# Kernel tuning notes

Measured on AMD Instinct MI355X. Metric: run time of the kernel, lower is better.

Reference implementation:

```python
import jax, jax.numpy as jnp
import numpy as np

N_NODES = 100000
N_EDGES = 1600000
D_IN = 128
D_HID = 128


def setup_inputs() -> dict:
    key = jax.random.key(0)
    ks = jax.random.split(key, 9)
    x = jax.random.normal(ks[0], (N_NODES, D_IN), dtype=jnp.float32)
    edge_index = jax.random.randint(ks[1], (2, N_EDGES), 0, N_NODES, dtype=jnp.int64)
    s = 1.0 / np.sqrt(D_IN)
    W0 = jax.random.uniform(ks[2], (D_IN, D_HID), jnp.float32, -s, s)
    W1 = jax.random.uniform(ks[3], (D_HID, D_HID), jnp.float32, -s, s)
    W2 = jax.random.uniform(ks[4], (D_HID, D_HID), jnp.float32, -s, s)
    b0 = jax.random.uniform(ks[5], (D_HID,), jnp.float32, -s, s)
    b1 = jax.random.uniform(ks[6], (D_HID,), jnp.float32, -s, s)
    b2 = jax.random.uniform(ks[7], (D_HID,), jnp.float32, -s, s)
    return {"x": x, "edge_index": edge_index,
            "W0": W0, "W1": W1, "W2": W2, "b0": b0, "b1": b1, "b2": b2}


def _gcn_norm(edge_index, num_nodes):
    # add self loops, compute symmetric normalization D^-1/2 (A+I) D^-1/2
    loop = jnp.arange(num_nodes, dtype=edge_index.dtype)
    src = jnp.concatenate([edge_index[0], loop])
    dst = jnp.concatenate([edge_index[1], loop])
    deg = jax.ops.segment_sum(jnp.ones_like(dst, dtype=jnp.float32), dst,
                              num_segments=num_nodes)
    dis = jnp.where(deg > 0, jax.lax.rsqrt(deg), 0.0)
    norm = dis[src] * dis[dst]  # [E+N]
    return src, dst, norm


def _gcn_conv(x, src, dst, norm, W, b, num_nodes):
    h = x @ W                           # [N, D]
    msg = h[src] * norm[:, None]        # [E+N, D]
    out = jax.ops.segment_sum(msg, dst, num_segments=num_nodes)
    return out + b


def reference(x, edge_index, W0, W1, W2, b0, b1, b2):
    n = x.shape[0]
    src, dst, norm = _gcn_norm(edge_index, n)
    h = jax.nn.relu(_gcn_conv(x, src, dst, norm, W0, b0, n))
    h = jax.nn.relu(_gcn_conv(h, src, dst, norm, W1, b1, n))
    h = jax.nn.relu(_gcn_conv(h, src, dst, norm, W2, b2, n))
    return jax.nn.log_softmax(h, axis=1)
```

## Files before the change

### kernel.cpp

```cpp
#include <hip/hip_runtime.h>
#include <cstdint>


#define D 128
#define NBMAX 800
#define ACHUNK 8192

typedef __attribute__((ext_vector_type(8))) short bf16x8;
typedef __attribute__((ext_vector_type(4))) float f32x4;

__device__ inline ushort f_to_bf(float f) {
    uint x = __float_as_uint(f);
    return (ushort)((x + 0x7fffu + ((x >> 16) & 1u)) >> 16);
}
__device__ inline uint pack_bf2(float a, float b) {
    return (uint)f_to_bf(a) | ((uint)f_to_bf(b) << 16);
}
__device__ inline float bf_lo(uint u) { return __uint_as_float(u << 16); }
__device__ inline float bf_hi(uint u) { return __uint_as_float(u & 0xffff0000u); }


__global__ void hist_pass(const int* __restrict__ ei, int* __restrict__ hist,
                          int E, int NB) {
    __shared__ int lh[NBMAX];
    for (int i = threadIdx.x; i < NB; i += 256) lh[i] = 0;
    __syncthreads();
    int e0 = blockIdx.x * ACHUNK;
    int e1 = min(e0 + ACHUNK, E);
    for (int e = e0 + threadIdx.x; e < e1; e += 256)
        atomicAdd(&lh[ei[(size_t)E + e] >> 7], 1);
    __syncthreads();
    int* hrow = hist + (size_t)blockIdx.x * NB;
    for (int i = threadIdx.x; i < NB; i += 256) hrow[i] = lh[i];
}

__global__ void col_scan(int* __restrict__ hist, int* __restrict__ btotal,
                         int B, int NB) {
    __shared__ int s[256];
    int g = blockIdx.x;
    int t = threadIdx.x;
    int v = (t < B) ? hist[(size_t)t * NB + g] : 0;
    s[t] = v;
    __syncthreads();
    for (int off = 1; off < 256; off <<= 1) {
        int u = (t >= off) ? s[t - off] : 0;
        __syncthreads();
        s[t] += u;
        __syncthreads();
    }
    if (t < B) hist[(size_t)t * NB + g] = s[t] - v;
    if (t == 255) btotal[g] = s[255];
}

__global__ void base_scan(const int* __restrict__ btotal, int* __restrict__ bbase,
                          int NB, int E) {
    __shared__ int s[1024];
    int t = threadIdx.x;
    int v = (t < NB) ? btotal[t] : 0;
    s[t] = v;
    __syncthreads();
    for (int off = 1; off < 1024; off <<= 1) {
        int u = (t >= off) ? s[t - off] : 0;
        __syncthreads();
        s[t] += u;
        __syncthreads();
    }
    if (t < NB) bbase[t] = s[t] - v;
    if (t == 0) bbase[NB] = E;
}

__global__ void scatter_pass(const int* __restrict__ ei, const int* __restrict__ hist,
                             const int* __restrict__ bbase, uint2* __restrict__ queue,
                             int E, int NB) {
    __shared__ int loff[NBMAX];
    const int* hrow = hist + (size_t)blockIdx.x * NB;
    for (int i = threadIdx.x; i < NB; i += 256) loff[i] = bbase[i] + hrow[i];
    __syncthreads();
    int e0 = blockIdx.x * ACHUNK;
    int e1 = min(e0 + ACHUNK, E);
    for (int e = e0 + threadIdx.x; e < e1; e += 256) {
        int d = ei[(size_t)E + e];
        int s = ei[e];
        int slot = atomicAdd(&loff[d >> 7], 1);
        queue[slot] = make_uint2((uint)d, (uint)s);
    }
}

__global__ void finalize_pass(const uint2* __restrict__ queue, const int* __restrict__ bbase,
                              int* __restrict__ rowptr, float* __restrict__ dis,
                              int* __restrict__ col, int N, int NB) {
    __shared__ int cnt[128], pre[128], run[128];
    int g = blockIdx.x;
    int t = threadIdx.x;
    int base = bbase[g], next = bbase[g + 1];
    if (t < 128) { cnt[t] = 0; run[t] = 0; }
    __syncthreads();
    for (int i = base + t; i < next; i += 256)
        atomicAdd(&cnt[queue[i].x & 127], 1);
    __syncthreads();
    if (t < 128) pre[t] = cnt[t];
    __syncthreads();
    for (int off = 1; off < 128; off <<= 1) {
        int u = (t < 128 && t >= off) ? pre[t - off] : 0;
        __syncthreads();
        if (t < 128) pre[t] += u;
        __syncthreads();
    }
    if (t < 128) {
        int node = (g << 7) + t;
        if (node < N) {
            rowptr[node] = base + pre[t] - cnt[t];
            dis[node] = rsqrtf((float)(cnt[t] + 1));
        }
    }
    if (g == NB - 1 && t == 0) rowptr[N] = next;
    __syncthreads();
    for (int i = base + t; i < next; i += 256) {
        uint2 e = queue[i];
        int idx = (int)(e.x & 127);
        int r = atomicAdd(&run[idx], 1);
        col[base + pre[idx] - cnt[idx] + r] = (int)e.y;
    }
}

__global__ void convert_w3(const float* __restrict__ W0, const float* __restrict__ W1,
                           const float* __restrict__ W2, ushort* __restrict__ Wt0,
                           ushort* __restrict__ Wt1, ushort* __restrict__ Wt2) {
    int which = blockIdx.x >> 6;
    int i = (blockIdx.x & 63) * 256 + threadIdx.x;
    const float* W = which == 0 ? W0 : (which == 1 ? W1 : W2);
    ushort* Wt = which == 0 ? Wt0 : (which == 1 ? Wt1 : Wt2);
    int k = i >> 7, nn = i & 127;
    Wt[nn * D + k] = f_to_bf(W[i]);
}

template <int F32IN>
__global__ __launch_bounds__(256)
void gemm_mfma(const void* __restrict__ Xv, const ushort* __restrict__ Wt,
               const float* __restrict__ dis, ushort* __restrict__ G, int n) {
    __shared__ ushort Bs[32 * 64 * 8];
    int tid = threadIdx.x;
    int wave = tid >> 6, lane = tid & 63;
    int lr = lane & 15, quad = lane >> 4;
    int rowbase = blockIdx.x * 128 + wave * 32;

    for (int s = tid; s < 2048; s += 256) {
        int g = s >> 6, l = s & 63;
        int kk = g >> 3, nt = g & 7;
        int srow = nt * 16 + (l & 15);
        int scol = kk * 32 + (l >> 4) * 8;
        ((uint4*)Bs)[s] = *(const uint4*)(Wt + srow * D + scol);
    }
    __syncthreads();

    int ar0 = min(rowbase + lr, n - 1);
    int ar1 = min(rowbase + 16 + lr, n - 1);

    f32x4 acc[2][8];
#pragma unroll
    for (int rt = 0; rt < 2; rt++)
#pragma unroll
        for (int nt = 0; nt < 8; nt++) acc[rt][nt] = (f32x4){0.f, 0.f, 0.f, 0.f};

#pragma unroll
    for (int kk = 0; kk < 4; kk++) {
        bf16x8 a0, a1;
        if (F32IN) {
            const float* X = (const float*)Xv;
            const float* p0 = X + (size_t)ar0 * D + kk * 32 + quad * 8;
            const float* p1 = X + (size_t)ar1 * D + kk * 32 + quad * 8;
            float4 u0 = ((const float4*)p0)[0], v0 = ((const float4*)p0)[1];
            float4 u1 = ((const float4*)p1)[0], v1 = ((const float4*)p1)[1];
            a0 = (bf16x8){(short)f_to_bf(u0.x), (short)f_to_bf(u0.y), (short)f_to_bf(u0.z), (short)f_to_bf(u0.w),
                          (short)f_to_bf(v0.x), (short)f_to_bf(v0.y), (short)f_to_bf(v0.z), (short)f_to_bf(v0.w)};
            a1 = (bf16x8){(short)f_to_bf(u1.x), (short)f_to_bf(u1.y), (short)f_to_bf(u1.z), (short)f_to_bf(u1.w),
                          (short)f_to_bf(v1.x), (short)f_to_bf(v1.y), (short)f_to_bf(v1.z), (short)f_to_bf(v1.w)};
        } else {
            const ushort* X = (const ushort*)Xv;
            a0 = ((const bf16x8*)(X + (size_t)ar0 * D))[kk * 4 + quad];
            a1 = ((const bf16x8*)(X + (size_t)ar1 * D))[kk * 4 + quad];
        }
#pragma unroll
        for (int nt = 0; nt < 8; nt++) {
            bf16x8 b = ((const bf16x8*)Bs)[(kk * 8 + nt) * 64 + lane];
            acc[0][nt] = __builtin_amdgcn_mfma_f32_16x16x32_bf16(a0, b, acc[0][nt], 0, 0, 0);
            acc[1][nt] = __builtin_amdgcn_mfma_f32_16x16x32_bf16(a1, b, acc[1][nt], 0, 0, 0);
        }
    }

#pragma unroll
    for (int rt = 0; rt < 2; rt++) {
#pragma unroll
        for (int r = 0; r < 4; r++) {
            int row = rowbase + rt * 16 + quad * 4 + r;
            if (row < n) {
                float dsc = dis[row];
#pragma unroll
                for (int nt = 0; nt < 8; nt++)
                    G[(size_t)row * D + nt * 16 + lr] = f_to_bf(dsc * acc[rt][nt][r]);
            }
        }
    }
}

template <int MODE>
__global__ __launch_bounds__(256)
void aggregate(const ushort* __restrict__ Gv, const float* __restrict__ dis,
               const int* __restrict__ rowptr, const int* __restrict__ col,
               const float* __restrict__ bias, void* __restrict__ outv, int n) {
    int node = blockIdx.x * 16 + (threadIdx.x >> 4);
    if (node >= n) return;
    int lane = threadIdx.x & 15;
    const uint4* base = (const uint4*)Gv;

    uint4 u = base[(size_t)node * 16 + lane];
    float a0 = bf_lo(u.x), a1 = bf_hi(u.x), a2 = bf_lo(u.y), a3 = bf_hi(u.y);
    float a4 = bf_lo(u.z), a5 = bf_hi(u.z), a6 = bf_lo(u.w), a7 = bf_hi(u.w);

    int beg = rowptr[node], end = rowptr[node + 1];
    int j = beg;
    for (; j + 8 <= end; j += 8) {
        uint4 v0 = base[(size_t)col[j + 0] * 16 + lane];
        uint4 v1 = base[(size_t)col[j + 1] * 16 + lane];
        uint4 v2 = base[(size_t)col[j + 2] * 16 + lane];
        uint4 v3 = base[(size_t)col[j + 3] * 16 + lane];
        uint4 v4 = base[(size_t)col[j + 4] * 16 + lane];
        uint4 v5 = base[(size_t)col[j + 5] * 16 + lane];
        uint4 v6 = base[(size_t)col[j + 6] * 16 + lane];
        uint4 v7 = base[(size_t)col[j + 7] * 16 + lane];
        a0 += bf_lo(v0.x) + bf_lo(v1.x) + bf_lo(v2.x) + bf_lo(v3.x)
            + bf_lo(v4.x) + bf_lo(v5.x) + bf_lo(v6.x) + bf_lo(v7.x);
        a1 += bf_hi(v0.x) + bf_hi(v1.x) + bf_hi(v2.x) + bf_hi(v3.x)
            + bf_hi(v4.x) + bf_hi(v5.x) + bf_hi(v6.x) + bf_hi(v7.x);
        a2 += bf_lo(v0.y) + bf_lo(v1.y) + bf_lo(v2.y) + bf_lo(v3.y)
            + bf_lo(v4.y) + bf_lo(v5.y) + bf_lo(v6.y) + bf_lo(v7.y);
        a3 += bf_hi(v0.y) + bf_hi(v1.y) + bf_hi(v2.y) + bf_hi(v3.y)
            + bf_hi(v4.y) + bf_hi(v5.y) + bf_hi(v6.y) + bf_hi(v7.y);
        a4 += bf_lo(v0.z) + bf_lo(v1.z) + bf_lo(v2.z) + bf_lo(v3.z)
            + bf_lo(v4.z) + bf_lo(v5.z) + bf_lo(v6.z) + bf_lo(v7.z);
        a5 += bf_hi(v0.z) + bf_hi(v1.z) + bf_hi(v2.z) + bf_hi(v3.z)
            + bf_hi(v4.z) + bf_hi(v5.z) + bf_hi(v6.z) + bf_hi(v7.z);
        a6 += bf_lo(v0.w) + bf_lo(v1.w) + bf_lo(v2.w) + bf_lo(v3.w)
            + bf_lo(v4.w) + bf_lo(v5.w) + bf_lo(v6.w) + bf_lo(v7.w);
        a7 += bf_hi(v0.w) + bf_hi(v1.w) + bf_hi(v2.w) + bf_hi(v3.w)
            + bf_hi(v4.w) + bf_hi(v5.w) + bf_hi(v6.w) + bf_hi(v7.w);
    }
    for (; j < end; j++) {
        uint4 v = base[(size_t)col[j] * 16 + lane];
        a0 += bf_lo(v.x); a1 += bf_hi(v.x); a2 += bf_lo(v.y); a3 += bf_hi(v.y);
        a4 += bf_lo(v.z); a5 += bf_hi(v.z); a6 += bf_lo(v.w); a7 += bf_hi(v.w);
    }

    float di = dis[node];
    float4 bA = ((const float4*)bias)[lane * 2];
    float4 bB = ((const float4*)bias)[lane * 2 + 1];
    a0 = fmaxf(di * a0 + bA.x, 0.f); a1 = fmaxf(di * a1 + bA.y, 0.f);
    a2 = fmaxf(di * a2 + bA.z, 0.f); a3 = fmaxf(di * a3 + bA.w, 0.f);
    a4 = fmaxf(di * a4 + bB.x, 0.f); a5 = fmaxf(di * a5 + bB.y, 0.f);
    a6 = fmaxf(di * a6 + bB.z, 0.f); a7 = fmaxf(di * a7 + bB.w, 0.f);

    if (MODE == 1) {
        float m = fmaxf(fmaxf(fmaxf(a0, a1), fmaxf(a2, a3)),
                        fmaxf(fmaxf(a4, a5), fmaxf(a6, a7)));
        for (int off = 8; off > 0; off >>= 1) m = fmaxf(m, __shfl_xor(m, off, 16));
        float e = __expf(a0 - m) + __expf(a1 - m) + __expf(a2 - m) + __expf(a3 - m)
                + __expf(a4 - m) + __expf(a5 - m) + __expf(a6 - m) + __expf(a7 - m);
        for (int off = 8; off > 0; off >>= 1) e += __shfl_xor(e, off, 16);
        float ls = m + __logf(e);
        ((float4*)outv)[(size_t)node * 32 + lane * 2]     = make_float4(a0 - ls, a1 - ls, a2 - ls, a3 - ls);
        ((float4*)outv)[(size_t)node * 32 + lane * 2 + 1] = make_float4(a4 - ls, a5 - ls, a6 - ls, a7 - ls);
    } else {
        ((uint4*)outv)[(size_t)node * 16 + lane] =
            make_uint4(pack_bf2(a0, a1), pack_bf2(a2, a3), pack_bf2(a4, a5), pack_bf2(a6, a7));
    }
}


static inline size_t align256(size_t x) { return (x + 255) & ~(size_t)255; }

extern "C" void kernel_launch(void* const* d_in, const int* in_sizes, int n_in,
                              void* d_out, int out_size, void* d_ws, size_t ws_size,
                              hipStream_t stream) {
    const float* x  = (const float*)d_in[0];
    const int*   ei = (const int*)d_in[1];
    const float* W0 = (const float*)d_in[2];
    const float* W1 = (const float*)d_in[3];
    const float* W2 = (const float*)d_in[4];
    const float* b0 = (const float*)d_in[5];
    const float* b1 = (const float*)d_in[6];
    const float* b2 = (const float*)d_in[7];
    float* out      = (float*)d_out;

    const int N = in_sizes[0] / D;
    const int E = in_sizes[1] / 2;

    const int NB = (N + 127) >> 7;
    const int B  = (E + ACHUNK - 1) / ACHUNK;

    char* ws = (char*)d_ws;
    size_t off = 0;
    float*  dis      = (float*)(ws + off);  off = align256(off + (size_t)N * 4);
    int*    rowptr   = (int*)(ws + off);    off = align256(off + ((size_t)N + 1) * 4);
    int*    hist     = (int*)(ws + off);    off = align256(off + (size_t)B * NB * 4);
    int*    btotal   = (int*)(ws + off);    off = align256(off + ((size_t)NB + 1) * 4);
    int*    bbase    = (int*)(ws + off);    off = align256(off + ((size_t)NB + 1) * 4);
    ushort* Wt0      = (ushort*)(ws + off); off = align256(off + (size_t)D * D * 2);
    ushort* Wt1      = (ushort*)(ws + off); off = align256(off + (size_t)D * D * 2);
    ushort* Wt2      = (ushort*)(ws + off); off = align256(off + (size_t)D * D * 2);
    int*    col      = (int*)(ws + off);    off = align256(off + (size_t)E * 4);
    ushort* xb       = (ushort*)(ws + off); off = align256(off + (size_t)N * D * 2);
    ushort* gA       = (ushort*)(ws + off); off = align256(off + (size_t)N * D * 2);
    ushort* hb       = (ushort*)d_out;
    uint2*  queue    = (uint2*)gA;
    (void)ws_size;

    hist_pass<<<B, 256, 0, stream>>>(ei, hist, E, NB);
    col_scan<<<NB, 256, 0, stream>>>(hist, btotal, B, NB);
    base_scan<<<1, 1024, 0, stream>>>(btotal, bbase, NB, E);
    scatter_pass<<<B, 256, 0, stream>>>(ei, hist, bbase, queue, E, NB);
    finalize_pass<<<NB, 256, 0, stream>>>(queue, bbase, rowptr, dis, col, N, NB);

    convert_w3<<<192, 256, 0, stream>>>(W0, W1, W2, Wt0, Wt1, Wt2);

    const int gemmBlocks = (N + 127) / 128;
    const int aggBlocks  = (N + 15) / 16;

    gemm_mfma<1><<<gemmBlocks, 256, 0, stream>>>(x, Wt0, dis, gA, N);
    aggregate<0><<<aggBlocks, 256, 0, stream>>>(gA, dis, rowptr, col, b0, hb, N);
    gemm_mfma<0><<<gemmBlocks, 256, 0, stream>>>(hb, Wt1, dis, gA, N);
    aggregate<0><<<aggBlocks, 256, 0, stream>>>(gA, dis, rowptr, col, b1, xb, N);
    gemm_mfma<0><<<gemmBlocks, 256, 0, stream>>>(xb, Wt2, dis, gA, N);
    aggregate<1><<<aggBlocks, 256, 0, stream>>>(gA, dis, rowptr, col, b2, out, N);
}
```

Measured before the change: 414.2 us.

## Build CSR with global atomic degree count and unordered per-node scatter

Replaces the five-kernel bucketed counting sort (histogram, column scan, base scan, bucket scatter, finalize) with three kernels: a global atomic degree count, a block-level scan that claims row ranges by atomic on a global counter, and a direct atomic scatter into col. Row ranges are stored as (begin, degree) pairs, so rows need not be contiguous in node order, and zeroing of the counters is folded into the weight-conversion kernel. This removes launches and the intermediate queue pass. In exchange it adds contention from global atomics, nondeterministic neighbor order within rows, and possibly poorer locality of col reads in aggregation.

```diff
diff --git a/kernel.cpp b/kernel.cpp
--- a/kernel.cpp
+++ b/kernel.cpp
@@ -3,8 +3,6 @@
 
 
 #define D 128
-#define NBMAX 800
-#define ACHUNK 8192
 
 typedef __attribute__((ext_vector_type(8))) short bf16x8;
 typedef __attribute__((ext_vector_type(4))) float f32x4;
@@ -20,27 +18,20 @@
 __device__ inline float bf_hi(uint u) { return __uint_as_float(u & 0xffff0000u); }
 
 
-__global__ void hist_pass(const int* __restrict__ ei, int* __restrict__ hist,
-                          int E, int NB) {
-    __shared__ int lh[NBMAX];
-    for (int i = threadIdx.x; i < NB; i += 256) lh[i] = 0;
-    __syncthreads();
-    int e0 = blockIdx.x * ACHUNK;
-    int e1 = min(e0 + ACHUNK, E);
-    for (int e = e0 + threadIdx.x; e < e1; e += 256)
-        atomicAdd(&lh[ei[(size_t)E + e] >> 7], 1);
-    __syncthreads();
-    int* hrow = hist + (size_t)blockIdx.x * NB;
-    for (int i = threadIdx.x; i < NB; i += 256) hrow[i] = lh[i];
-}
-
-__global__ void col_scan(int* __restrict__ hist, int* __restrict__ btotal,
-                         int B, int NB) {
+__global__ void deg_count(const int* __restrict__ ei, int* __restrict__ cnt, int E) {
+    int stride = gridDim.x * blockDim.x;
+    for (int e = blockIdx.x * blockDim.x + threadIdx.x; e < E; e += stride)
+        atomicAdd(&cnt[ei[(size_t)E + e]], 1);
+}
+
+__global__ void assign_base(int* __restrict__ cnt, int2* __restrict__ bd,
+                            float* __restrict__ dis, int N) {
     __shared__ int s[256];
-    int g = blockIdx.x;
+    __shared__ int base;
     int t = threadIdx.x;
-    int v = (t < B) ? hist[(size_t)t * NB + g] : 0;
-    s[t] = v;
+    int i = blockIdx.x * 256 + t;
+    int d = (i < N) ? cnt[i] : 0;
+    s[t] = d;
     __syncthreads();
     for (int off = 1; off < 256; off <<= 1) {
         int u = (t >= off) ? s[t - off] : 0;
@@ -48,84 +39,33 @@
         s[t] += u;
         __syncthreads();
     }
-    if (t < B) hist[(size_t)t * NB + g] = s[t] - v;
-    if (t == 255) btotal[g] = s[255];
-}
-
-__global__ void base_scan(const int* __restrict__ btotal, int* __restrict__ bbase,
-                          int NB, int E) {
-    __shared__ int s[1024];
-    int t = threadIdx.x;
-    int v = (t < NB) ? btotal[t] : 0;
-    s[t] = v;
+    if (t == 255) base = atomicAdd(&cnt[N], s[255]);
     __syncthreads();
-    for (int off = 1; off < 1024; off <<= 1) {
-        int u = (t >= off) ? s[t - off] : 0;
-        __syncthreads();
-        s[t] += u;
-        __syncthreads();
-    }
-    if (t < NB) bbase[t] = s[t] - v;
-    if (t == 0) bbase[NB] = E;
-}
-
-__global__ void scatter_pass(const int* __restrict__ ei, const int* __restrict__ hist,
-                             const int* __restrict__ bbase, uint2* __restrict__ queue,
-                             int E, int NB) {
-    __shared__ int loff[NBMAX];
-    const int* hrow = hist + (size_t)blockIdx.x * NB;
-    for (int i = threadIdx.x; i < NB; i += 256) loff[i] = bbase[i] + hrow[i];
-    __syncthreads();
-    int e0 = blockIdx.x * ACHUNK;
-    int e1 = min(e0 + ACHUNK, E);
-    for (int e = e0 + threadIdx.x; e < e1; e += 256) {
+    if (i < N) {
+        int beg = base + s[t] - d;
+        bd[i] = make_int2(beg, d);
+        cnt[i] = beg;
+        dis[i] = rsqrtf((float)(d + 1));
+    }
+}
+
+__global__ void scatter_csr(const int* __restrict__ ei, int* __restrict__ cur,
+                            int* __restrict__ col, int E) {
+    int stride = gridDim.x * blockDim.x;
+    for (int e = blockIdx.x * blockDim.x + threadIdx.x; e < E; e += stride) {
         int d = ei[(size_t)E + e];
         int s = ei[e];
-        int slot = atomicAdd(&loff[d >> 7], 1);
-        queue[slot] = make_uint2((uint)d, (uint)s);
-    }
-}
-
-__global__ void finalize_pass(const uint2* __restrict__ queue, const int* __restrict__ bbase,
-                              int* __restrict__ rowptr, float* __restrict__ dis,
-                              int* __restrict__ col, int N, int NB) {
-    __shared__ int cnt[128], pre[128], run[128];
-    int g = blockIdx.x;
-    int t = threadIdx.x;
-    int base = bbase[g], next = bbase[g + 1];
-    if (t < 128) { cnt[t] = 0; run[t] = 0; }
-    __syncthreads();
-    for (int i = base + t; i < next; i += 256)
-        atomicAdd(&cnt[queue[i].x & 127], 1);
-    __syncthreads();
-    if (t < 128) pre[t] = cnt[t];
-    __syncthreads();
-    for (int off = 1; off < 128; off <<= 1) {
-        int u = (t < 128 && t >= off) ? pre[t - off] : 0;
-        __syncthreads();
-        if (t < 128) pre[t] += u;
-        __syncthreads();
-    }
-    if (t < 128) {
-        int node = (g << 7) + t;
-        if (node < N) {
-            rowptr[node] = base + pre[t] - cnt[t];
-            dis[node] = rsqrtf((float)(cnt[t] + 1));
-        }
-    }
-    if (g == NB - 1 && t == 0) rowptr[N] = next;
-    __syncthreads();
-    for (int i = base + t; i < next; i += 256) {
-        uint2 e = queue[i];
-        int idx = (int)(e.x & 127);
-        int r = atomicAdd(&run[idx], 1);
-        col[base + pre[idx] - cnt[idx] + r] = (int)e.y;
+        int slot = atomicAdd(&cur[d], 1);
+        col[slot] = s;
     }
 }
 
 __global__ void convert_w3(const float* __restrict__ W0, const float* __restrict__ W1,
                            const float* __restrict__ W2, ushort* __restrict__ Wt0,
-                           ushort* __restrict__ Wt1, ushort* __restrict__ Wt2) {
+                           ushort* __restrict__ Wt1, ushort* __restrict__ Wt2,
+                           int* __restrict__ cnt, int N) {
+    int gid = blockIdx.x * 256 + threadIdx.x;
+    for (int z = gid; z <= N; z += 192 * 256) cnt[z] = 0;
     int which = blockIdx.x >> 6;
     int i = (blockIdx.x & 63) * 256 + threadIdx.x;
     const float* W = which == 0 ? W0 : (which == 1 ? W1 : W2);
@@ -206,7 +146,7 @@
 template <int MODE>
 __global__ __launch_bounds__(256)
 void aggregate(const ushort* __restrict__ Gv, const float* __restrict__ dis,
-               const int* __restrict__ rowptr, const int* __restrict__ col,
+               const int2* __restrict__ bd, const int* __restrict__ col,
                const float* __restrict__ bias, void* __restrict__ outv, int n) {
     int node = blockIdx.x * 16 + (threadIdx.x >> 4);
     if (node >= n) return;
@@ -217,7 +157,8 @@
     float a0 = bf_lo(u.x), a1 = bf_hi(u.x), a2 = bf_lo(u.y), a3 = bf_hi(u.y);
     float a4 = bf_lo(u.z), a5 = bf_hi(u.z), a6 = bf_lo(u.w), a7 = bf_hi(u.w);
 
-    int beg = rowptr[node], end = rowptr[node + 1];
+    int2 be = bd[node];
+    int beg = be.x, end = be.x + be.y;
     int j = beg;
     for (; j + 8 <= end; j += 8) {
         uint4 v0 = base[(size_t)col[j + 0] * 16 + lane];
@@ -294,16 +235,11 @@
     const int N = in_sizes[0] / D;
     const int E = in_sizes[1] / 2;
 
-    const int NB = (N + 127) >> 7;
-    const int B  = (E + ACHUNK - 1) / ACHUNK;
-
     char* ws = (char*)d_ws;
     size_t off = 0;
     float*  dis      = (float*)(ws + off);  off = align256(off + (size_t)N * 4);
-    int*    rowptr   = (int*)(ws + off);    off = align256(off + ((size_t)N + 1) * 4);
-    int*    hist     = (int*)(ws + off);    off = align256(off + (size_t)B * NB * 4);
-    int*    btotal   = (int*)(ws + off);    off = align256(off + ((size_t)NB + 1) * 4);
-    int*    bbase    = (int*)(ws + off);    off = align256(off + ((size_t)NB + 1) * 4);
+    int*    cnt      = (int*)(ws + off);    off = align256(off + ((size_t)N + 1) * 4);
+    int2*   bd       = (int2*)(ws + off);   off = align256(off + (size_t)N * 8);
     ushort* Wt0      = (ushort*)(ws + off); off = align256(off + (size_t)D * D * 2);
     ushort* Wt1      = (ushort*)(ws + off); off = align256(off + (size_t)D * D * 2);
     ushort* Wt2      = (ushort*)(ws + off); off = align256(off + (size_t)D * D * 2);
@@ -311,24 +247,21 @@
     ushort* xb       = (ushort*)(ws + off); off = align256(off + (size_t)N * D * 2);
     ushort* gA       = (ushort*)(ws + off); off = align256(off + (size_t)N * D * 2);
     ushort* hb       = (ushort*)d_out;
-    uint2*  queue    = (uint2*)gA;
     (void)ws_size;
 
-    hist_pass<<<B, 256, 0, stream>>>(ei, hist, E, NB);
-    col_scan<<<NB, 256, 0, stream>>>(hist, btotal, B, NB);
-    base_scan<<<1, 1024, 0, stream>>>(btotal, bbase, NB, E);
-    scatter_pass<<<B, 256, 0, stream>>>(ei, hist, bbase, queue, E, NB);
-    finalize_pass<<<NB, 256, 0, stream>>>(queue, bbase, rowptr, dis, col, N, NB);
-
-    convert_w3<<<192, 256, 0, stream>>>(W0, W1, W2, Wt0, Wt1, Wt2);
+    convert_w3<<<192, 256, 0, stream>>>(W0, W1, W2, Wt0, Wt1, Wt2, cnt, N);
+
+    deg_count<<<1024, 256, 0, stream>>>(ei, cnt, E);
+    assign_base<<<(N + 255) / 256, 256, 0, stream>>>(cnt, bd, dis, N);
+    scatter_csr<<<2048, 256, 0, stream>>>(ei, cnt, col, E);
 
     const int gemmBlocks = (N + 127) / 128;
     const int aggBlocks  = (N + 15) / 16;
 
     gemm_mfma<1><<<gemmBlocks, 256, 0, stream>>>(x, Wt0, dis, gA, N);
-    aggregate<0><<<aggBlocks, 256, 0, stream>>>(gA, dis, rowptr, col, b0, hb, N);
+    aggregate<0><<<aggBlocks, 256, 0, stream>>>(gA, dis, bd, col, b0, hb, N);
     gemm_mfma<0><<<gemmBlocks, 256, 0, stream>>>(hb, Wt1, dis, gA, N);
-    aggregate<0><<<aggBlocks, 256, 0, stream>>>(gA, dis, rowptr, col, b1, xb, N);
+    aggregate<0><<<aggBlocks, 256, 0, stream>>>(gA, dis, bd, col, b1, xb, N);
     gemm_mfma<0><<<gemmBlocks, 256, 0, stream>>>(xb, Wt2, dis, gA, N);
-    aggregate<1><<<aggBlocks, 256, 0, stream>>>(gA, dis, rowptr, col, b2, out, N);
-}
+    aggregate<1><<<aggBlocks, 256, 0, stream>>>(gA, dis, bd, col, b2, out, N);
+}
```

Result: slower. 565.4 us (+36.5%).

## Fuse aggregation with next-layer GEMM and streamline CSR build

Applied to the files above, without the earlier changes.

Adds an agg_gemm kernel that gathers neighbor rows, applies bias and ReLU, then multiplies the 16-row tile by the next weight matrix with MFMA in shared memory. This removes two standalone GEMM launches and the round trip of hidden activations through global memory. CSR construction is also trimmed: base_scan is replaced by an atomic cursor in col_scan, queue entries are packed to 32 bits, finalize stages each bucket in LDS, and rowptr becomes (begin,count) pairs. In exchange, every 16-node block reloads the full 32KB weight matrix into LDS, bucket bases come out in nondeterministic order, and the packed format assumes source ids fit in 17 bits.

```diff
diff --git a/kernel.cpp b/kernel.cpp
--- a/kernel.cpp
+++ b/kernel.cpp
@@ -5,6 +5,7 @@
 #define D 128
 #define NBMAX 800
 #define ACHUNK 8192
+#define QCAP 4608
 
 typedef __attribute__((ext_vector_type(8))) short bf16x8;
 typedef __attribute__((ext_vector_type(4))) float f32x4;
@@ -21,8 +22,9 @@
 
 
 __global__ void hist_pass(const int* __restrict__ ei, int* __restrict__ hist,
-                          int E, int NB) {
+                          int* __restrict__ cursor, int E, int NB) {
     __shared__ int lh[NBMAX];
+    if (blockIdx.x == 0 && threadIdx.x == 0) *cursor = 0;
     for (int i = threadIdx.x; i < NB; i += 256) lh[i] = 0;
     __syncthreads();
     int e0 = blockIdx.x * ACHUNK;
@@ -35,6 +37,7 @@
 }
 
 __global__ void col_scan(int* __restrict__ hist, int* __restrict__ btotal,
+                         int* __restrict__ bbase, int* __restrict__ cursor,
                          int B, int NB) {
     __shared__ int s[256];
     int g = blockIdx.x;
@@ -49,28 +52,14 @@
         __syncthreads();
     }
     if (t < B) hist[(size_t)t * NB + g] = s[t] - v;
-    if (t == 255) btotal[g] = s[255];
-}
-
-__global__ void base_scan(const int* __restrict__ btotal, int* __restrict__ bbase,
-                          int NB, int E) {
-    __shared__ int s[1024];
-    int t = threadIdx.x;
-    int v = (t < NB) ? btotal[t] : 0;
-    s[t] = v;
-    __syncthreads();
-    for (int off = 1; off < 1024; off <<= 1) {
-        int u = (t >= off) ? s[t - off] : 0;
-        __syncthreads();
-        s[t] += u;
-        __syncthreads();
-    }
-    if (t < NB) bbase[t] = s[t] - v;
-    if (t == 0) bbase[NB] = E;
+    if (t == 255) {
+        btotal[g] = s[255];
+        bbase[g] = atomicAdd(cursor, s[255]);
+    }
 }
 
 __global__ void scatter_pass(const int* __restrict__ ei, const int* __restrict__ hist,
-                             const int* __restrict__ bbase, uint2* __restrict__ queue,
+                             const int* __restrict__ bbase, uint* __restrict__ queue,
                              int E, int NB) {
     __shared__ int loff[NBMAX];
     const int* hrow = hist + (size_t)blockIdx.x * NB;
@@ -82,21 +71,26 @@
         int d = ei[(size_t)E + e];
         int s = ei[e];
         int slot = atomicAdd(&loff[d >> 7], 1);
-        queue[slot] = make_uint2((uint)d, (uint)s);
-    }
-}
-
-__global__ void finalize_pass(const uint2* __restrict__ queue, const int* __restrict__ bbase,
-                              int* __restrict__ rowptr, float* __restrict__ dis,
-                              int* __restrict__ col, int N, int NB) {
+        queue[slot] = ((uint)(d & 127) << 17) | (uint)s;
+    }
+}
+
+__global__ void finalize_pass(const uint* __restrict__ queue, const int* __restrict__ bbase,
+                              const int* __restrict__ btotal, int2* __restrict__ bd,
+                              float* __restrict__ dis, int* __restrict__ col, int N) {
+    __shared__ uint qs[QCAP];
     __shared__ int cnt[128], pre[128], run[128];
     int g = blockIdx.x;
     int t = threadIdx.x;
-    int base = bbase[g], next = bbase[g + 1];
+    int base = bbase[g], m = btotal[g];
+    bool fits = (m <= QCAP);
     if (t < 128) { cnt[t] = 0; run[t] = 0; }
     __syncthreads();
-    for (int i = base + t; i < next; i += 256)
-        atomicAdd(&cnt[queue[i].x & 127], 1);
+    for (int i = t; i < m; i += 256) {
+        uint e = queue[base + i];
+        if (fits) qs[i] = e;
+        atomicAdd(&cnt[e >> 17], 1);
+    }
     __syncthreads();
     if (t < 128) pre[t] = cnt[t];
     __syncthreads();
@@ -109,17 +103,16 @@
     if (t < 128) {
         int node = (g << 7) + t;
         if (node < N) {
-            rowptr[node] = base + pre[t] - cnt[t];
+            bd[node] = make_int2(base + pre[t] - cnt[t], cnt[t]);
             dis[node] = rsqrtf((float)(cnt[t] + 1));
         }
     }
-    if (g == NB - 1 && t == 0) rowptr[N] = next;
-    __syncthreads();
-    for (int i = base + t; i < next; i += 256) {
-        uint2 e = queue[i];
-        int idx = (int)(e.x & 127);
+    __syncthreads();
+    for (int i = t; i < m; i += 256) {
+        uint e = fits ? qs[i] : queue[base + i];
+        int idx = (int)(e >> 17);
         int r = atomicAdd(&run[idx], 1);
-        col[base + pre[idx] - cnt[idx] + r] = (int)e.y;
+        col[base + pre[idx] - cnt[idx] + r] = (int)(e & 0x1FFFFu);
     }
 }
 
@@ -203,10 +196,115 @@
     }
 }
 
+__global__ __launch_bounds__(256)
+void agg_gemm(const ushort* __restrict__ Gv, const float* __restrict__ dis,
+              const int2* __restrict__ bd, const int* __restrict__ col,
+              const float* __restrict__ bias, const ushort* __restrict__ Wt,
+              ushort* __restrict__ Gout, int n) {
+    __shared__ ushort Bs[32 * 64 * 8];
+    __shared__ ushort As[16 * 128];
+    int tid = threadIdx.x;
+    int r16 = tid >> 4;
+    int lane16 = tid & 15;
+    int node = blockIdx.x * 16 + r16;
+
+    for (int s = tid; s < 2048; s += 256) {
+        int g = s >> 6, l = s & 63;
+        int kk = g >> 3, nt = g & 7;
+        int srow = nt * 16 + (l & 15);
+        int scol = kk * 32 + (l >> 4) * 8;
+        ((uint4*)Bs)[s] = *(const uint4*)(Wt + srow * D + scol);
+    }
+
+    float a0 = 0.f, a1 = 0.f, a2 = 0.f, a3 = 0.f,
+          a4 = 0.f, a5 = 0.f, a6 = 0.f, a7 = 0.f;
+    if (node < n) {
+        const uint4* base = (const uint4*)Gv;
+        uint4 u = base[(size_t)node * 16 + lane16];
+        a0 = bf_lo(u.x); a1 = bf_hi(u.x); a2 = bf_lo(u.y); a3 = bf_hi(u.y);
+        a4 = bf_lo(u.z); a5 = bf_hi(u.z); a6 = bf_lo(u.w); a7 = bf_hi(u.w);
+
+        int2 be = bd[node];
+        int beg = be.x, end = be.x + be.y;
+        int j = beg;
+        for (; j + 8 <= end; j += 8) {
+            uint4 v0 = base[(size_t)col[j + 0] * 16 + lane16];
+            uint4 v1 = base[(size_t)col[j + 1] * 16 + lane16];
+            uint4 v2 = base[(size_t)col[j + 2] * 16 + lane16];
+            uint4 v3 = base[(size_t)col[j + 3] * 16 + lane16];
+            uint4 v4 = base[(size_t)col[j + 4] * 16 + lane16];
+            uint4 v5 = base[(size_t)col[j + 5] * 16 + lane16];
+            uint4 v6 = base[(size_t)col[j + 6] * 16 + lane16];
+            uint4 v7 = base[(size_t)col[j + 7] * 16 + lane16];
+            a0 += bf_lo(v0.x) + bf_lo(v1.x) + bf_lo(v2.x) + bf_lo(v3.x)
+                + bf_lo(v4.x) + bf_lo(v5.x) + bf_lo(v6.x) + bf_lo(v7.x);
+            a1 += bf_hi(v0.x) + bf_hi(v1.x) + bf_hi(v2.x) + bf_hi(v3.x)
+                + bf_hi(v4.x) + bf_hi(v5.x) + bf_hi(v6.x) + bf_hi(v7.x);
+            a2 += bf_lo(v0.y) + bf_lo(v1.y) + bf_lo(v2.y) + bf_lo(v3.y)
+                + bf_lo(v4.y) + bf_lo(v5.y) + bf_lo(v6.y) + bf_lo(v7.y);
+            a3 += bf_hi(v0.y) + bf_hi(v1.y) + bf_hi(v2.y) + bf_hi(v3.y)
+                + bf_hi(v4.y) + bf_hi(v5.y) + bf_hi(v6.y) + bf_hi(v7.y);
+            a4 += bf_lo(v0.z) + bf_lo(v1.z) + bf_lo(v2.z) + bf_lo(v3.z)
+                + bf_lo(v4.z) + bf_lo(v5.z) + bf_lo(v6.z) + bf_lo(v7.z);
+            a5 += bf_hi(v0.z) + bf_hi(v1.z) + bf_hi(v2.z) + bf_hi(v3.z)
+                + bf_hi(v4.z) + bf_hi(v5.z) + bf_hi(v6.z) + bf_hi(v7.z);
+            a6 += bf_lo(v0.w) + bf_lo(v1.w) + bf_lo(v2.w) + bf_lo(v3.w)
+                + bf_lo(v4.w) + bf_lo(v5.w) + bf_lo(v6.w) + bf_lo(v7.w);
+            a7 += bf_hi(v0.w) + bf_hi(v1.w) + bf_hi(v2.w) + bf_hi(v3.w)
+                + bf_hi(v4.w) + bf_hi(v5.w) + bf_hi(v6.w) + bf_hi(v7.w);
+        }
+        for (; j < end; j++) {
+            uint4 v = base[(size_t)col[j] * 16 + lane16];
+            a0 += bf_lo(v.x); a1 += bf_hi(v.x); a2 += bf_lo(v.y); a3 += bf_hi(v.y);
+            a4 += bf_lo(v.z); a5 += bf_hi(v.z); a6 += bf_lo(v.w); a7 += bf_hi(v.w);
+        }
+
+        float di = dis[node];
+        float4 bA = ((const float4*)bias)[lane16 * 2];
+        float4 bB = ((const float4*)bias)[lane16 * 2 + 1];
+        a0 = fmaxf(di * a0 + bA.x, 0.f); a1 = fmaxf(di * a1 + bA.y, 0.f);
+        a2 = fmaxf(di * a2 + bA.z, 0.f); a3 = fmaxf(di * a3 + bA.w, 0.f);
+        a4 = fmaxf(di * a4 + bB.x, 0.f); a5 = fmaxf(di * a5 + bB.y, 0.f);
+        a6 = fmaxf(di * a6 + bB.z, 0.f); a7 = fmaxf(di * a7 + bB.w, 0.f);
+    }
+
+    {
+        uint4 packed = make_uint4(pack_bf2(a0, a1), pack_bf2(a2, a3),
+                                  pack_bf2(a4, a5), pack_bf2(a6, a7));
+        uint woff = ((uint)(r16 * 256 + lane16 * 16)) ^ ((uint)(r16 & 7) << 4);
+        *(uint4*)((char*)As + woff) = packed;
+    }
+    __syncthreads();
+
+    int wave = tid >> 6, lane = tid & 63;
+    int lr = lane & 15, quad = lane >> 4;
+    f32x4 acc0 = (f32x4){0.f, 0.f, 0.f, 0.f};
+    f32x4 acc1 = (f32x4){0.f, 0.f, 0.f, 0.f};
+#pragma unroll
+    for (int kk = 0; kk < 4; kk++) {
+        uint roff = ((uint)(lr * 256 + (kk * 4 + quad) * 16)) ^ ((uint)(lr & 7) << 4);
+        bf16x8 a = *(const bf16x8*)((const char*)As + roff);
+        bf16x8 b0 = ((const bf16x8*)Bs)[(kk * 8 + wave * 2 + 0) * 64 + lane];
+        bf16x8 b1 = ((const bf16x8*)Bs)[(kk * 8 + wave * 2 + 1) * 64 + lane];
+        acc0 = __builtin_amdgcn_mfma_f32_16x16x32_bf16(a, b0, acc0, 0, 0, 0);
+        acc1 = __builtin_amdgcn_mfma_f32_16x16x32_bf16(a, b1, acc1, 0, 0, 0);
+    }
+
+#pragma unroll
+    for (int r = 0; r < 4; r++) {
+        int row = blockIdx.x * 16 + quad * 4 + r;
+        if (row < n) {
+            float dsc = dis[row];
+            Gout[(size_t)row * D + (wave * 2 + 0) * 16 + lr] = f_to_bf(dsc * acc0[r]);
+            Gout[(size_t)row * D + (wave * 2 + 1) * 16 + lr] = f_to_bf(dsc * acc1[r]);
+        }
+    }
+}
+
 template <int MODE>
 __global__ __launch_bounds__(256)
 void aggregate(const ushort* __restrict__ Gv, const float* __restrict__ dis,
-               const int* __restrict__ rowptr, const int* __restrict__ col,
+               const int2* __restrict__ bd, const int* __restrict__ col,
                const float* __restrict__ bias, void* __restrict__ outv, int n) {
     int node = blockIdx.x * 16 + (threadIdx.x >> 4);
     if (node >= n) return;
@@ -217,7 +315,8 @@
     float a0 = bf_lo(u.x), a1 = bf_hi(u.x), a2 = bf_lo(u.y), a3 = bf_hi(u.y);
     float a4 = bf_lo(u.z), a5 = bf_hi(u.z), a6 = bf_lo(u.w), a7 = bf_hi(u.w);
 
-    int beg = rowptr[node], end = rowptr[node + 1];
+    int2 be = bd[node];
+    int beg = be.x, end = be.x + be.y;
     int j = beg;
     for (; j + 8 <= end; j += 8) {
         uint4 v0 = base[(size_t)col[j + 0] * 16 + lane];
@@ -300,35 +399,33 @@
     char* ws = (char*)d_ws;
     size_t off = 0;
     float*  dis      = (float*)(ws + off);  off = align256(off + (size_t)N * 4);
-    int*    rowptr   = (int*)(ws + off);    off = align256(off + ((size_t)N + 1) * 4);
+    int2*   bd       = (int2*)(ws + off);   off = align256(off + (size_t)N * 8);
     int*    hist     = (int*)(ws + off);    off = align256(off + (size_t)B * NB * 4);
-    int*    btotal   = (int*)(ws + off);    off = align256(off + ((size_t)NB + 1) * 4);
-    int*    bbase    = (int*)(ws + off);    off = align256(off + ((size_t)NB + 1) * 4);
+    int*    btotal   = (int*)(ws + off);    off = align256(off + (size_t)NB * 4);
+    int*    bbase    = (int*)(ws + off);    off = align256(off + (size_t)NB * 4);
+    int*    cursor   = (int*)(ws + off);    off = align256(off + 4);
     ushort* Wt0      = (ushort*)(ws + off); off = align256(off + (size_t)D * D * 2);
     ushort* Wt1      = (ushort*)(ws + off); off = align256(off + (size_t)D * D * 2);
     ushort* Wt2      = (ushort*)(ws + off); off = align256(off + (size_t)D * D * 2);
     int*    col      = (int*)(ws + off);    off = align256(off + (size_t)E * 4);
-    ushort* xb       = (ushort*)(ws + off); off = align256(off + (size_t)N * D * 2);
     ushort* gA       = (ushort*)(ws + off); off = align256(off + (size_t)N * D * 2);
-    ushort* hb       = (ushort*)d_out;
-    uint2*  queue    = (uint2*)gA;
+    ushort* gB       = (ushort*)(ws + off); off = align256(off + (size_t)N * D * 2);
+    ushort* g0       = (ushort*)d_out;
+    uint*   queue    = (uint*)gA;
     (void)ws_size;
 
-    hist_pass<<<B, 256, 0, stream>>>(ei, hist, E, NB);
-    col_scan<<<NB, 256, 0, stream>>>(hist, btotal, B, NB);
-    base_scan<<<1, 1024, 0, stream>>>(btotal, bbase, NB, E);
+    hist_pass<<<B, 256, 0, stream>>>(ei, hist, cursor, E, NB);
+    col_scan<<<NB, 256, 0, stream>>>(hist, btotal, bbase, cursor, B, NB);
     scatter_pass<<<B, 256, 0, stream>>>(ei, hist, bbase, queue, E, NB);
-    finalize_pass<<<NB, 256, 0, stream>>>(queue, bbase, rowptr, dis, col, N, NB);
+    finalize_pass<<<NB, 256, 0, stream>>>(queue, bbase, btotal, bd, dis, col, N);
 
     convert_w3<<<192, 256, 0, stream>>>(W0, W1, W2, Wt0, Wt1, Wt2);
 
     const int gemmBlocks = (N + 127) / 128;
-    const int aggBlocks  = (N + 15) / 16;
-
-    gemm_mfma<1><<<gemmBlocks, 256, 0, stream>>>(x, Wt0, dis, gA, N);
-    aggregate<0><<<aggBlocks, 256, 0, stream>>>(gA, dis, rowptr, col, b0, hb, N);
-    gemm_mfma<0><<<gemmBlocks, 256, 0, stream>>>(hb, Wt1, dis, gA, N);
-    aggregate<0><<<aggBlocks, 256, 0, stream>>>(gA, dis, rowptr, col, b1, xb, N);
-    gemm_mfma<0><<<gemmBlocks, 256, 0, stream>>>(xb, Wt2, dis, gA, N);
-    aggregate<1><<<aggBlocks, 256, 0, stream>>>(gA, dis, rowptr, col, b2, out, N);
-}
+    const int fuseBlocks = (N + 15) / 16;
+
+    gemm_mfma<1><<<gemmBlocks, 256, 0, stream>>>(x, Wt0, dis, g0, N);
+    agg_gemm<<<fuseBlocks, 256, 0, stream>>>(g0, dis, bd, col, b0, Wt1, gA, N);
+    agg_gemm<<<fuseBlocks, 256, 0, stream>>>(gA, dis, bd, col, b1, Wt2, gB, N);
+    aggregate<1><<<fuseBlocks, 256, 0, stream>>>(gB, dis, bd, col, b2, out, N);
+}
```

New measurement: 433.8 us. 1.05x slower.

## Fuse CSR build and weight conversion into one cooperative grid-synced kernel

Applied to the files above, without the earlier changes.

Replaces the five CSR-construction launches and the weight conversion with a single cooperative kernel that uses grid.sync between histogram, scan, scatter and finalize phases. Bucket bases now come from an atomic cursor instead of a separate scan. Queue entries are packed into 32-bit words and staged in shared memory during finalize, and rows are described by (begin, count) pairs instead of a rowptr array. This is meant to cut launch overhead and memory traffic in the preprocessing stage, at the cost of relying on cooperative launch, with the old multi-kernel path kept as a fallback.

```diff
diff --git a/kernel.cpp b/kernel.cpp
--- a/kernel.cpp
+++ b/kernel.cpp
@@ -1,10 +1,14 @@
 #include <hip/hip_runtime.h>
+#include <hip/hip_cooperative_groups.h>
 #include <cstdint>
 
 
 #define D 128
 #define NBMAX 800
-#define ACHUNK 8192
+#define QCAP 4608
+#define CB 256
+
+namespace cg = cooperative_groups;
 
 typedef __attribute__((ext_vector_type(8))) short bf16x8;
 typedef __attribute__((ext_vector_type(4))) float f32x4;
@@ -20,13 +24,124 @@
 __device__ inline float bf_hi(uint u) { return __uint_as_float(u & 0xffff0000u); }
 
 
+__global__ __launch_bounds__(256)
+void csr_build(const int* __restrict__ ei,
+               const float* __restrict__ W0, const float* __restrict__ W1,
+               const float* __restrict__ W2, ushort* __restrict__ Wt0,
+               ushort* __restrict__ Wt1, ushort* __restrict__ Wt2,
+               int* __restrict__ hist, int* __restrict__ btotal,
+               int* __restrict__ bbase, int* __restrict__ cursor,
+               uint* __restrict__ queue, int2* __restrict__ bd,
+               float* __restrict__ dis, int* __restrict__ col,
+               int E, int N, int NB) {
+    cg::grid_group grid = cg::this_grid();
+    __shared__ int lh[NBMAX];
+    __shared__ int s256[256];
+    __shared__ uint qs[QCAP];
+    __shared__ int cnt[128], pre[128], run[128];
+
+    int b = blockIdx.x, t = threadIdx.x;
+    int CE = (E + CB - 1) / CB;
+
+    {
+        int i = b * 256 + t;
+        if (i < 3 * D * D) {
+            int which = i >> 14, r = i & 16383;
+            const float* W = which == 0 ? W0 : (which == 1 ? W1 : W2);
+            ushort* Wt = which == 0 ? Wt0 : (which == 1 ? Wt1 : Wt2);
+            Wt[(r & 127) * D + (r >> 7)] = f_to_bf(W[r]);
+        }
+        if (b == 0 && t == 0) *cursor = 0;
+        for (int i2 = t; i2 < NB; i2 += 256) lh[i2] = 0;
+        __syncthreads();
+        int e0 = b * CE, e1 = min(e0 + CE, E);
+        for (int e = e0 + t; e < e1; e += 256)
+            atomicAdd(&lh[ei[(size_t)E + e] >> 7], 1);
+        __syncthreads();
+        int* hrow = hist + (size_t)b * NB;
+        for (int i2 = t; i2 < NB; i2 += 256) hrow[i2] = lh[i2];
+    }
+    grid.sync();
+
+    for (int g = b; g < NB; g += CB) {
+        int v = hist[(size_t)t * NB + g];
+        s256[t] = v;
+        __syncthreads();
+        for (int off = 1; off < 256; off <<= 1) {
+            int u = (t >= off) ? s256[t - off] : 0;
+            __syncthreads();
+            s256[t] += u;
+            __syncthreads();
+        }
+        hist[(size_t)t * NB + g] = s256[t] - v;
+        if (t == 255) {
+            btotal[g] = s256[255];
+            bbase[g] = atomicAdd(cursor, s256[255]);
+        }
+        __syncthreads();
+    }
+    grid.sync();
+
+    {
+        const int* hrow = hist + (size_t)b * NB;
+        for (int i = t; i < NB; i += 256) lh[i] = bbase[i] + hrow[i];
+        __syncthreads();
+        int e0 = b * CE, e1 = min(e0 + CE, E);
+        for (int e = e0 + t; e < e1; e += 256) {
+            int d = ei[(size_t)E + e];
+            int s = ei[e];
+            int slot = atomicAdd(&lh[d >> 7], 1);
+            queue[slot] = ((uint)(d & 127) << 17) | (uint)s;
+        }
+    }
+    grid.sync();
+
+    for (int g = b; g < NB; g += CB) {
+        int base = bbase[g], m = btotal[g];
+        bool fits = (m <= QCAP);
+        if (t < 128) { cnt[t] = 0; run[t] = 0; }
+        __syncthreads();
+        for (int i = t; i < m; i += 256) {
+            uint e = queue[base + i];
+            if (fits) qs[i] = e;
+            atomicAdd(&cnt[e >> 17], 1);
+        }
+        __syncthreads();
+        if (t < 128) pre[t] = cnt[t];
+        __syncthreads();
+        for (int off = 1; off < 128; off <<= 1) {
+            int u = (t < 128 && t >= off) ? pre[t - off] : 0;
+            __syncthreads();
+            if (t < 128) pre[t] += u;
+            __syncthreads();
+        }
+        if (t < 128) {
+            int node = (g << 7) + t;
+            if (node < N) {
+                bd[node] = make_int2(base + pre[t] - cnt[t], cnt[t]);
+                dis[node] = rsqrtf((float)(cnt[t] + 1));
+            }
+        }
+        __syncthreads();
+        for (int i = t; i < m; i += 256) {
+            uint e = fits ? qs[i] : queue[base + i];
+            int idx = (int)(e >> 17);
+            int r = atomicAdd(&run[idx], 1);
+            col[base + pre[idx] - cnt[idx] + r] = (int)(e & 0x1FFFFu);
+        }
+        __syncthreads();
+    }
+}
+
+
 __global__ void hist_pass(const int* __restrict__ ei, int* __restrict__ hist,
-                          int E, int NB) {
+                          int* __restrict__ cursor, int E, int NB) {
     __shared__ int lh[NBMAX];
+    if (blockIdx.x == 0 && threadIdx.x == 0) *cursor = 0;
     for (int i = threadIdx.x; i < NB; i += 256) lh[i] = 0;
     __syncthreads();
-    int e0 = blockIdx.x * ACHUNK;
-    int e1 = min(e0 + ACHUNK, E);
+    int CE = (E + CB - 1) / CB;
+    int e0 = blockIdx.x * CE, e1 = min(e0 + CE, E);
     for (int e = e0 + threadIdx.x; e < e1; e += 256)
         atomicAdd(&lh[ei[(size_t)E + e] >> 7], 1);
     __syncthreads();
@@ -35,11 +150,10 @@
 }
 
 __global__ void col_scan(int* __restrict__ hist, int* __restrict__ btotal,
-                         int B, int NB) {
+                         int* __restrict__ bbase, int* __restrict__ cursor, int NB) {
     __shared__ int s[256];
-    int g = blockIdx.x;
-    int t = threadIdx.x;
-    int v = (t < B) ? hist[(size_t)t * NB + g] : 0;
+    int g = blockIdx.x, t = threadIdx.x;
+    int v = hist[(size_t)t * NB + g];
     s[t] = v;
     __syncthreads();
     for (int off = 1; off < 256; off <<= 1) {
@@ -48,55 +162,42 @@
         s[t] += u;
         __syncthreads();
     }
-    if (t < B) hist[(size_t)t * NB + g] = s[t] - v;
-    if (t == 255) btotal[g] = s[255];
-}
-
-__global__ void base_scan(const int* __restrict__ btotal, int* __restrict__ bbase,
-                          int NB, int E) {
-    __shared__ int s[1024];
-    int t = threadIdx.x;
-    int v = (t < NB) ? btotal[t] : 0;
-    s[t] = v;
-    __syncthreads();
-    for (int off = 1; off < 1024; off <<= 1) {
-        int u = (t >= off) ? s[t - off] : 0;
-        __syncthreads();
-        s[t] += u;
-        __syncthreads();
-    }
-    if (t < NB) bbase[t] = s[t] - v;
-    if (t == 0) bbase[NB] = E;
+    hist[(size_t)t * NB + g] = s[t] - v;
+    if (t == 255) { btotal[g] = s[255]; bbase[g] = atomicAdd(cursor, s[255]); }
 }
 
 __global__ void scatter_pass(const int* __restrict__ ei, const int* __restrict__ hist,
-                             const int* __restrict__ bbase, uint2* __restrict__ queue,
+                             const int* __restrict__ bbase, uint* __restrict__ queue,
                              int E, int NB) {
     __shared__ int loff[NBMAX];
     const int* hrow = hist + (size_t)blockIdx.x * NB;
     for (int i = threadIdx.x; i < NB; i += 256) loff[i] = bbase[i] + hrow[i];
     __syncthreads();
-    int e0 = blockIdx.x * ACHUNK;
-    int e1 = min(e0 + ACHUNK, E);
+    int CE = (E + CB - 1) / CB;
+    int e0 = blockIdx.x * CE, e1 = min(e0 + CE, E);
     for (int e = e0 + threadIdx.x; e < e1; e += 256) {
         int d = ei[(size_t)E + e];
         int s = ei[e];
         int slot = atomicAdd(&loff[d >> 7], 1);
-        queue[slot] = make_uint2((uint)d, (uint)s);
-    }
-}
-
-__global__ void finalize_pass(const uint2* __restrict__ queue, const int* __restrict__ bbase,
-                              int* __restrict__ rowptr, float* __restrict__ dis,
-                              int* __restrict__ col, int N, int NB) {
+        queue[slot] = ((uint)(d & 127) << 17) | (uint)s;
+    }
+}
+
+__global__ void finalize_pass(const uint* __restrict__ queue, const int* __restrict__ bbase,
+                              const int* __restrict__ btotal, int2* __restrict__ bd,
+                              float* __restrict__ dis, int* __restrict__ col, int N) {
+    __shared__ uint qs[QCAP];
     __shared__ int cnt[128], pre[128], run[128];
-    int g = blockIdx.x;
-    int t = threadIdx.x;
-    int base = bbase[g], next = bbase[g + 1];
+    int g = blockIdx.x, t = threadIdx.x;
+    int base = bbase[g], m = btotal[g];
+    bool fits = (m <= QCAP);
     if (t < 128) { cnt[t] = 0; run[t] = 0; }
     __syncthreads();
-    for (int i = base + t; i < next; i += 256)
-        atomicAdd(&cnt[queue[i].x & 127], 1);
+    for (int i = t; i < m; i += 256) {
+        uint e = queue[base + i];
+        if (fits) qs[i] = e;
+        atomicAdd(&cnt[e >> 17], 1);
+    }
     __syncthreads();
     if (t < 128) pre[t] = cnt[t];
     __syncthreads();
@@ -109,17 +210,16 @@
     if (t < 128) {
         int node = (g << 7) + t;
         if (node < N) {
-            rowptr[node] = base + pre[t] - cnt[t];
+            bd[node] = make_int2(base + pre[t] - cnt[t], cnt[t]);
             dis[node] = rsqrtf((float)(cnt[t] + 1));
         }
     }
-    if (g == NB - 1 && t == 0) rowptr[N] = next;
-    __syncthreads();
-    for (int i = base + t; i < next; i += 256) {
-        uint2 e = queue[i];
-        int idx = (int)(e.x & 127);
+    __syncthreads();
+    for (int i = t; i < m; i += 256) {
+        uint e = fits ? qs[i] : queue[base + i];
+        int idx = (int)(e >> 17);
         int r = atomicAdd(&run[idx], 1);
-        col[base + pre[idx] - cnt[idx] + r] = (int)e.y;
+        col[base + pre[idx] - cnt[idx] + r] = (int)(e & 0x1FFFFu);
     }
 }
 
@@ -206,7 +306,7 @@
 template <int MODE>
 __global__ __launch_bounds__(256)
 void aggregate(const ushort* __restrict__ Gv, const float* __restrict__ dis,
-               const int* __restrict__ rowptr, const int* __restrict__ col,
+               const int2* __restrict__ bd, const int* __restrict__ col,
                const float* __restrict__ bias, void* __restrict__ outv, int n) {
     int node = blockIdx.x * 16 + (threadIdx.x >> 4);
     if (node >= n) return;
@@ -217,7 +317,8 @@
     float a0 = bf_lo(u.x), a1 = bf_hi(u.x), a2 = bf_lo(u.y), a3 = bf_hi(u.y);
     float a4 = bf_lo(u.z), a5 = bf_hi(u.z), a6 = bf_lo(u.w), a7 = bf_hi(u.w);
 
-    int beg = rowptr[node], end = rowptr[node + 1];
+    int2 be = bd[node];
+    int beg = be.x, end = be.x + be.y;
     int j = beg;
     for (; j + 8 <= end; j += 8) {
         uint4 v0 = base[(size_t)col[j + 0] * 16 + lane];
@@ -293,42 +394,54 @@
 
     const int N = in_sizes[0] / D;
     const int E = in_sizes[1] / 2;
-
     const int NB = (N + 127) >> 7;
-    const int B  = (E + ACHUNK - 1) / ACHUNK;
 
     char* ws = (char*)d_ws;
     size_t off = 0;
     float*  dis      = (float*)(ws + off);  off = align256(off + (size_t)N * 4);
-    int*    rowptr   = (int*)(ws + off);    off = align256(off + ((size_t)N + 1) * 4);
-    int*    hist     = (int*)(ws + off);    off = align256(off + (size_t)B * NB * 4);
-    int*    btotal   = (int*)(ws + off);    off = align256(off + ((size_t)NB + 1) * 4);
-    int*    bbase    = (int*)(ws + off);    off = align256(off + ((size_t)NB + 1) * 4);
+    int2*   bd       = (int2*)(ws + off);   off = align256(off + (size_t)N * 8);
+    int*    hist     = (int*)(ws + off);    off = align256(off + (size_t)CB * NB * 4);
+    int*    btotal   = (int*)(ws + off);    off = align256(off + (size_t)NB * 4);
+    int*    bbase    = (int*)(ws + off);    off = align256(off + (size_t)NB * 4);
+    int*    cursor   = (int*)(ws + off);    off = align256(off + 4);
     ushort* Wt0      = (ushort*)(ws + off); off = align256(off + (size_t)D * D * 2);
     ushort* Wt1      = (ushort*)(ws + off); off = align256(off + (size_t)D * D * 2);
     ushort* Wt2      = (ushort*)(ws + off); off = align256(off + (size_t)D * D * 2);
     int*    col      = (int*)(ws + off);    off = align256(off + (size_t)E * 4);
-    ushort* xb       = (ushort*)(ws + off); off = align256(off + (size_t)N * D * 2);
-    ushort* gA       = (ushort*)(ws + off); off = align256(off + (size_t)N * D * 2);
-    ushort* hb       = (ushort*)d_out;
-    uint2*  queue    = (uint2*)gA;
+    ushort* bufA     = (ushort*)(ws + off); off = align256(off + (size_t)N * D * 2);
+    ushort* bufB     = (ushort*)(ws + off); off = align256(off + (size_t)N * D * 2);
+    ushort* dhead    = (ushort*)d_out;
+    uint*   queue    = (uint*)bufA;
     (void)ws_size;
 
-    hist_pass<<<B, 256, 0, stream>>>(ei, hist, E, NB);
-    col_scan<<<NB, 256, 0, stream>>>(hist, btotal, B, NB);
-    base_scan<<<1, 1024, 0, stream>>>(btotal, bbase, NB, E);
-    scatter_pass<<<B, 256, 0, stream>>>(ei, hist, bbase, queue, E, NB);
-    finalize_pass<<<NB, 256, 0, stream>>>(queue, bbase, rowptr, dis, col, N, NB);
-
-    convert_w3<<<192, 256, 0, stream>>>(W0, W1, W2, Wt0, Wt1, Wt2);
+    {
+        const int* ei_ = ei; const float *W0_ = W0, *W1_ = W1, *W2_ = W2;
+        ushort *Wt0_ = Wt0, *Wt1_ = Wt1, *Wt2_ = Wt2;
+        int *hist_ = hist, *btotal_ = btotal, *bbase_ = bbase, *cursor_ = cursor;
+        uint* queue_ = queue; int2* bd_ = bd; float* dis_ = dis; int* col_ = col;
+        int E_ = E, N_ = N, NB_ = NB;
+        void* params[] = {&ei_, &W0_, &W1_, &W2_, &Wt0_, &Wt1_, &Wt2_,
+                          &hist_, &btotal_, &bbase_, &cursor_, &queue_,
+                          &bd_, &dis_, &col_, &E_, &N_, &NB_};
+        hipError_t cerr = hipLaunchCooperativeKernel((void*)csr_build,
+                                                     dim3(CB), dim3(256),
+                                                     params, 0, stream);
+        if (cerr != hipSuccess) {
+            hist_pass<<<CB, 256, 0, stream>>>(ei, hist, cursor, E, NB);
+            col_scan<<<NB, 256, 0, stream>>>(hist, btotal, bbase, cursor, NB);
+            scatter_pass<<<CB, 256, 0, stream>>>(ei, hist, bbase, queue, E, NB);
+            finalize_pass<<<NB, 256, 0, stream>>>(queue, bbase, btotal, bd, dis, col, N);
+            convert_w3<<<192, 256, 0, stream>>>(W0, W1, W2, Wt0, Wt1, Wt2);
+        }
+    }
 
     const int gemmBlocks = (N + 127) / 128;
     const int aggBlocks  = (N + 15) / 16;
 
-    gemm_mfma<1><<<gemmBlocks, 256, 0, stream>>>(x, Wt0, dis, gA, N);
-    aggregate<0><<<aggBlocks, 256, 0, stream>>>(gA, dis, rowptr, col, b0, hb, N);
-    gemm_mfma<0><<<gemmBlocks, 256, 0, stream>>>(hb, Wt1, dis, gA, N);
-    aggregate<0><<<aggBlocks, 256, 0, stream>>>(gA, dis, rowptr, col, b1, xb, N);
-    gemm_mfma<0><<<gemmBlocks, 256, 0, stream>>>(xb, Wt2, dis, gA, N);
-    aggregate<1><<<aggBlocks, 256, 0, stream>>>(gA, dis, rowptr, col, b2, out, N);
-}
+    gemm_mfma<1><<<gemmBlocks, 256, 0, stream>>>(x, Wt0, dis, dhead, N);
+    aggregate<0><<<aggBlocks, 256, 0, stream>>>(dhead, dis, bd, col, b0, bufA, N);
+    gemm_mfma<0><<<gemmBlocks, 256, 0, stream>>>(bufA, Wt1, dis, bufB, N);
+    aggregate<0><<<aggBlocks, 256, 0, stream>>>(bufB, dis, bd, col, b1, dhead, N);
+    gemm_mfma<0><<<gemmBlocks, 256, 0, stream>>>(dhead, Wt2, dis, bufA, N);
+    aggregate<1><<<aggBlocks, 256, 0, stream>>>(bufA, dis, bd, col, b2, out, N);
+}
```

Result: slower. 536.7 us (+29.6%).
